# Kernel optimization log

Hardware: AMD Instinct MI355X
Metric: run time of the kernel (lower is better)

The kernel has to match this reference:

```python
import jax, jax.numpy as jnp
import numpy as np

NEG_SLOPE_GAT = 0.2    # PyG GATConv default negative_slope
NEG_SLOPE_ACT = 0.01   # F.leaky_relu default
D_DIRECTIONS = 4       # len(target): message directions per variable (uniform in this setup)
GAT_HEADS = 4


def gru_cell(x, h, Wih, Whh, bih, bhh):
    # torch.nn.GRUCell math; Wih [3H, in], Whh [3H, H]
    gi = x @ Wih.T + bih
    gh = h @ Whh.T + bhh
    ir, iz, inn = jnp.split(gi, 3, axis=1)
    hr, hz, hn = jnp.split(gh, 3, axis=1)
    r = jax.nn.sigmoid(ir + hr)
    z = jax.nn.sigmoid(iz + hz)
    n = jnp.tanh(inn + r * hn)
    return (1.0 - z) * n + z * h


def gat_conv(x, W, a_src, a_dst, bias, src, dst, heads, concat):
    # PyG GATConv (self-loops already included in src/dst)
    N = x.shape[0]
    C = W.shape[1] // heads
    h = (x @ W).reshape(N, heads, C)
    as_ = jnp.einsum('nhc,hc->nh', h, a_src)
    ad = jnp.einsum('nhc,hc->nh', h, a_dst)
    e = jax.nn.leaky_relu(as_[src] + ad[dst], NEG_SLOPE_GAT)  # [E, heads]
    m = jax.ops.segment_max(e, dst, num_segments=N)
    ex = jnp.exp(e - m[dst])
    den = jax.ops.segment_sum(ex, dst, num_segments=N)
    alpha = ex / den[dst]
    out = jax.ops.segment_sum(h[src] * alpha[:, :, None], dst, num_segments=N)
    if concat:
        return out.reshape(N, heads * C) + bias
    return out.mean(axis=1) + bias


def setup_inputs():
    key = jax.random.key(0)
    ki = iter(jax.random.split(key, 64))
    nk = lambda: next(ki)
    Nx, A, B = 100000, 50000, 50000
    IC, PD = 16, 3
    GH = IC - PD  # gru hidden = 13
    E, M, G, L, H, OC = 2000000, 1024, 1024, 4, 4, 32
    Ntot = Nx + A + B

    def p(*shape):
        return jax.random.normal(nk(), shape, jnp.float32) * 0.05

    inp = {}
    inp['x'] = jax.random.normal(nk(), (Nx, IC), jnp.float32)
    inp['edge_index'] = jax.random.randint(nk(), (2, E), 0, Ntot)
    inp['ass_to_sum_msg'] = jax.random.normal(nk(), (A, 1), jnp.float32)
    inp['ass_to_sum_hidden'] = jax.random.normal(nk(), (A, GH), jnp.float32)
    inp['sum_to_ass_msg'] = jax.random.normal(nk(), (B, 1), jnp.float32)
    inp['sum_to_ass_hidden'] = jax.random.normal(nk(), (B, GH), jnp.float32)
    inp['prefix'] = jax.random.normal(nk(), (A + B, PD), jnp.float32)
    inp['function_node_idxes'] = jax.random.randint(nk(), (M,), 0, Ntot)
    # regularized neighbor_idx_info: group g has direction idx=group_idx[g], src list group_src[g]
    # with idx at position 0 (out_i == 0) and no other entry equal to idx.
    gidx = jax.random.randint(nk(), (G,), 0, M)
    gs = jax.random.randint(nk(), (G, L), 0, M)
    rest = jnp.where(gs[:, 1:] == gidx[:, None], (gidx[:, None] + 1) % M, gs[:, 1:])
    inp['group_idx'] = gidx
    inp['group_src'] = jnp.concatenate([gidx[:, None], rest], axis=1)
    # GRU params
    for g in ('gru1', 'gru2'):
        inp[g + '_Wih'] = p(3 * GH, 1)
        inp[g + '_Whh'] = p(3 * GH, GH)
        inp[g + '_bih'] = p(3 * GH)
        inp[g + '_bhh'] = p(3 * GH)
    # GATConv params (W stored [in, heads*out], used as x @ W)
    inp['W1'] = p(IC, 32); inp['asrc1'] = p(4, 8); inp['adst1'] = p(4, 8); inp['b1'] = p(32)
    inp['W2'] = p(32, 32); inp['asrc2'] = p(4, 8); inp['adst2'] = p(4, 8); inp['b2'] = p(32)
    inp['W3'] = p(32, 32); inp['asrc3'] = p(4, 8); inp['adst3'] = p(4, 8); inp['b3'] = p(32)
    inp['W4'] = p(32, 4 * OC); inp['asrc4'] = p(4, OC); inp['adst4'] = p(4, OC); inp['b4'] = p(OC)
    # Attention heads: Wq/Wk [H, OC, OC] (applied as v @ Wq[h]), Ws [H, 2*OC], bs [H]
    inp['Wq'] = p(H, OC, OC); inp['Wk'] = p(H, OC, OC); inp['Ws'] = p(H, 2 * OC); inp['bs'] = p(H)
    return inp


def reference(x, edge_index, ass_to_sum_msg, ass_to_sum_hidden, sum_to_ass_msg,
              sum_to_ass_hidden, prefix, function_node_idxes, group_idx, group_src,
              gru1_Wih, gru1_Whh, gru1_bih, gru1_bhh,
              gru2_Wih, gru2_Whh, gru2_bih, gru2_bhh,
              W1, asrc1, adst1, b1, W2, asrc2, adst2, b2,
              W3, asrc3, adst3, b3, W4, asrc4, adst4, b4,
              Wq, Wk, Ws, bs):
    h1 = gru_cell(ass_to_sum_msg, ass_to_sum_hidden, gru1_Wih, gru1_Whh, gru1_bih, gru1_bhh)
    h2 = gru_cell(sum_to_ass_msg, sum_to_ass_hidden, gru2_Wih, gru2_Whh, gru2_bih, gru2_bhh)
    hidden = jnp.concatenate([h1, h2], axis=0)
    hidden = jnp.concatenate([prefix, hidden], axis=1)
    xx = jnp.concatenate([x, hidden], axis=0)
    N = xx.shape[0]
    loop = jnp.arange(N)
    src = jnp.concatenate([edge_index[0], loop])  # add self loops (PyG default)
    dst = jnp.concatenate([edge_index[1], loop])
    xx = jax.nn.leaky_relu(gat_conv(xx, W1, asrc1, adst1, b1, src, dst, GAT_HEADS, True), NEG_SLOPE_ACT)
    xx = jax.nn.leaky_relu(gat_conv(xx, W2, asrc2, adst2, b2, src, dst, GAT_HEADS, True), NEG_SLOPE_ACT)
    xx = jax.nn.leaky_relu(gat_conv(xx, W3, asrc3, adst3, b3, src, dst, GAT_HEADS, True), NEG_SLOPE_ACT)
    xx = jax.nn.leaky_relu(gat_conv(xx, W4, asrc4, adst4, b4, src, dst, GAT_HEADS, False), NEG_SLOPE_ACT)
    pooling = xx[function_node_idxes]  # [M, OC]
    hdim = pooling.shape[1]
    # score(i,j,h) = sigmoid((pooling_i @ Wq_h) . ws_q_h + (pooling_j @ Wk_h) . ws_k_h + bs_h)
    # (associativity: equals sigmoid(score_proj(cat([q_proj, k_proj]))) of the original)
    Vq = jnp.einsum('hdo,ho->hd', Wq, Ws[:, :hdim])
    Vk = jnp.einsum('hdo,ho->hd', Wk, Ws[:, hdim:])
    sq = pooling @ Vq.T  # [M, H]
    sk = pooling @ Vk.T  # [M, H]
    scores = jax.nn.sigmoid(sq[:, None, :] + sk[None, :, :] + bs)  # [M, M, H]; flat n -> (n//M, n%M)
    idx = group_idx
    nbr = group_src[:, 1:]  # idx itself sits at position 0 and is removed
    gathered = scores[idx[:, None], nbr]  # [G, L-1, H]
    trg = scores[idx, idx]                # [G, H]
    score_sum = gathered.mean(axis=1)
    tw = jax.nn.softmax(jnp.stack([score_sum, trg], axis=0), axis=0)  # [2, G, H]
    w = jax.nn.softmax(gathered, axis=1) * tw[0][:, None, :] * (D_DIRECTIONS - 1)
    weights = jnp.concatenate([tw[1][:, None, :], w], axis=1)  # [G, L, H] (out_i == 0)
    return weights, h1, h2
```

## Files before the change

### kernel.cpp

```cpp
#include <hip/hip_runtime.h>
#include <hip/hip_bf16.h>

#define NXD   100000
#define AROWS 50000
#define NND   200000
#define EED   2000000
#define ETOT  2200000
#define GHD   13
#define MMD   1024

#define OUT_H1 16384
#define OUT_H2 (16384 + AROWS * GHD)

#define NB    196
#define BSH   10
#define CAP   16000
#define TILE  4096

#define PREP_BIN   538
#define PREP_ASM   7422
#define PREP_GRU   392
#define FEAT_BLK   1563

typedef __hip_bfloat16 bf16;
typedef unsigned int uvec4 __attribute__((ext_vector_type(4)));

__device__ __forceinline__ float bf2f(bf16 v) { return __bfloat162float(v); }
__device__ __forceinline__ float sigm(float x) { return 1.f / (1.f + __expf(-x)); }
__device__ __forceinline__ float tanhfast(float x) {
    x = fminf(15.f, fmaxf(-15.f, x));
    float t = __expf(-2.f * x);
    return (1.f - t) / (1.f + t);
}
__device__ __forceinline__ float lrelu(float x, float s) { return x > 0.f ? x : s * x; }

__device__ __forceinline__ unsigned short f2bf_bits(float v) {
    bf16 b = __float2bfloat16(v);
    return *reinterpret_cast<unsigned short*>(&b);
}
__device__ __forceinline__ float bflo(unsigned int u) { return __uint_as_float((u & 0xFFFFu) << 16); }
__device__ __forceinline__ float bfhi(unsigned int u) { return __uint_as_float(u & 0xFFFF0000u); }

__device__ __forceinline__ float loadF(const void* p, size_t i, int f32) {
    return f32 ? ((const float*)p)[i] : bf2f(((const bf16*)p)[i]);
}
__device__ __forceinline__ void storeF(void* p, size_t i, float v, int f32) {
    if (f32) ((float*)p)[i] = v;
    else ((bf16*)p)[i] = __float2bfloat16(v);
}

__device__ __forceinline__ int flag_from_x(const void* xp, int tid, int* fl) {
    if (tid < 64) {
        const unsigned short* u = (const unsigned short*)xp;
        unsigned short b = u[tid * 2];
        int e = (b >> 7) & 0xFF;
        int viol = (e == 0xFF) || (e < 64) || (e > 190);
        unsigned long long mask = __ballot(viol != 0);
        if (tid == 0) *fl = (__popcll(mask) > 8) ? 1 : 0;
    }
    __syncthreads();
    return *fl;
}

__global__ void prep_kernel(const void* __restrict__ x, const void* __restrict__ prefix,
                            const void* __restrict__ msg1, const void* __restrict__ hid1,
                            const void* __restrict__ Wih1, const void* __restrict__ Whh1,
                            const void* __restrict__ bih1, const void* __restrict__ bhh1,
                            const void* __restrict__ msg2, const void* __restrict__ hid2,
                            const void* __restrict__ Wih2, const void* __restrict__ Whh2,
                            const void* __restrict__ bih2, const void* __restrict__ bhh2,
                            void* __restrict__ dout, bf16* __restrict__ bufA,
                            const int* __restrict__ src_e, const int* __restrict__ dst_e,
                            int* __restrict__ gtail, unsigned int* __restrict__ stage) {
    __shared__ int hist[NB];
    __shared__ int base[NB];
    __shared__ int cur[NB];
    __shared__ float WhhL[39 * 13], WihL[39], bihL[39], bhhL[39];
    __shared__ int fl;
    int bid = blockIdx.x, tid = threadIdx.x;
    if (bid < PREP_BIN) {
        for (int i = tid; i < NB; i += 256) hist[i] = 0;
        __syncthreads();
        int t0 = bid * TILE;
        int tend = t0 + TILE; if (tend > ETOT) tend = ETOT;
        for (int t = t0 + tid; t < tend; t += 256) {
            int d = (t < EED) ? dst_e[t] : (t - EED);
            atomicAdd(&hist[d >> BSH], 1);
        }
        __syncthreads();
        for (int i = tid; i < NB; i += 256) {
            int c = hist[i];
            base[i] = (c > 0) ? atomicAdd(&gtail[i], c) : 0;
            cur[i] = 0;
        }
        __syncthreads();
        for (int t = t0 + tid; t < tend; t += 256) {
            int s, d;
            if (t < EED) { s = src_e[t]; d = dst_e[t]; } else { s = d = t - EED; }
            int b = d >> BSH;
            int p = base[b] + atomicAdd(&cur[b], 1);
            if (p < CAP)
                stage[(size_t)b * CAP + p] = ((unsigned int)(d & 1023) << 18) | (unsigned int)s;
        }
    } else if (bid < PREP_BIN + PREP_ASM) {
        int f = flag_from_x(x, tid, &fl);
        int t = (bid - PREP_BIN) * 256 + tid;
        if (t < NXD * 16) {
            bufA[t] = __float2bfloat16(loadF(x, t, f));
        } else {
            int u = t - NXD * 16;
            if (u < NXD * 3) {
                int r = u / 3, c = u - r * 3;
                bufA[(size_t)(NXD + r) * 16 + c] = __float2bfloat16(loadF(prefix, u, f));
            }
        }
    } else {
        int f = flag_from_x(x, tid, &fl);
        int vb = bid - PREP_BIN - PREP_ASM;
        int which = vb >= 196;
        const void* msg = which ? msg2 : msg1;
        const void* hid = which ? hid2 : hid1;
        const void* Wih = which ? Wih2 : Wih1;
        const void* Whh = which ? Whh2 : Whh1;
        const void* bih = which ? bih2 : bih1;
        const void* bhh = which ? bhh2 : bhh1;
        size_t houtbase = which ? (size_t)OUT_H2 : (size_t)OUT_H1;
        int rowbase = which ? AROWS : 0;
        int blk = vb - (which ? 196 : 0);
        for (int i = tid; i < 39 * 13; i += 256) WhhL[i] = loadF(Whh, i, f);
        if (tid < 39) { WihL[tid] = loadF(Wih, tid, f); bihL[tid] = loadF(bih, tid, f); bhhL[tid] = loadF(bhh, tid, f); }
        __syncthreads();
        int n = blk * 256 + tid;
        if (n >= AROWS) return;
        float xv = loadF(msg, n, f);
        float h[GHD];
#pragma unroll
        for (int k = 0; k < GHD; k++) h[k] = loadF(hid, n * GHD + k, f);
#pragma unroll
        for (int k = 0; k < GHD; k++) {
            float gir = fmaf(xv, WihL[k],      bihL[k]);
            float giz = fmaf(xv, WihL[13 + k], bihL[13 + k]);
            float gin = fmaf(xv, WihL[26 + k], bihL[26 + k]);
            float ghr = bhhL[k], ghz = bhhL[13 + k], ghn = bhhL[26 + k];
#pragma unroll
            for (int q = 0; q < GHD; q++) {
                ghr = fmaf(h[q], WhhL[k * 13 + q],        ghr);
                ghz = fmaf(h[q], WhhL[(13 + k) * 13 + q], ghz);
                ghn = fmaf(h[q], WhhL[(26 + k) * 13 + q], ghn);
            }
            float r = sigm(gir + ghr);
            float z = sigm(giz + ghz);
            float nn = tanhfast(gin + r * ghn);
            float o = (1.f - z) * nn + z * h[k];
            storeF(dout, houtbase + (size_t)n * GHD + k, o, f);
            bufA[(size_t)(NXD + rowbase + n) * 16 + 3 + k] = __float2bfloat16(o);
        }
    }
}

template <int K>
__device__ __forceinline__ void feat_body(const bf16* __restrict__ xx,
                                          const void* __restrict__ W,
                                          bf16* __restrict__ hbuf, int f,
                                          int vbid, int tid) {
    int j = tid & 31;
    float Wc[K];
#pragma unroll
    for (int k = 0; k < K; k++) Wc[k] = loadF(W, k * 32 + j, f);
    int half = vbid * 8 + (tid >> 5);
    if (half >= NND / 16) return;
    int n0 = half * 16;
#pragma unroll 4
    for (int n = n0; n < n0 + 16; n++) {
        const uvec4* xr4 = (const uvec4*)(xx + (size_t)n * K);
        float v = 0.f;
#pragma unroll
        for (int q = 0; q < K / 8; q++) {
            uvec4 u = xr4[q];
            v = fmaf(bflo(u.x), Wc[q * 8 + 0], v);
            v = fmaf(bfhi(u.x), Wc[q * 8 + 1], v);
            v = fmaf(bflo(u.y), Wc[q * 8 + 2], v);
            v = fmaf(bfhi(u.y), Wc[q * 8 + 3], v);
            v = fmaf(bflo(u.z), Wc[q * 8 + 4], v);
            v = fmaf(bfhi(u.z), Wc[q * 8 + 5], v);
            v = fmaf(bflo(u.w), Wc[q * 8 + 6], v);
            v = fmaf(bfhi(u.w), Wc[q * 8 + 7], v);
        }
        hbuf[(size_t)n * 32 + j] = __float2bfloat16(v);
    }
}

__global__ void mid_kernel(const unsigned int* __restrict__ stage, const int* __restrict__ gtail,
                           int* __restrict__ offs, int* __restrict__ csr, int* __restrict__ order,
                           const bf16* __restrict__ xx, const void* __restrict__ W,
                           bf16* __restrict__ hbuf, const void* __restrict__ x) {
    __shared__ int cnt[1024];
    __shared__ int loc[1024];
    __shared__ int cur[1024];
    __shared__ int lds[256];
    __shared__ int dh[64];
    __shared__ int fl;
    int bid = blockIdx.x, tid = threadIdx.x;
    if (bid >= NB) {
        int f = flag_from_x(x, tid, &fl);
        feat_body<16>(xx, W, hbuf, f, bid - NB, tid);
        return;
    }
    int b = bid;
    int v = (tid < NB) ? gtail[tid] : 0;
    lds[tid] = v; __syncthreads();
    for (int off = 1; off < 256; off <<= 1) {
        int t2 = (tid >= off) ? lds[tid - off] : 0;
        __syncthreads();
        lds[tid] += t2;
        __syncthreads();
    }
    __shared__ int ebs;
    if (tid == b) ebs = lds[tid] - v;
    __syncthreads();
    int eb = ebs;
    int nE = gtail[b]; if (nE > CAP) nE = CAP;
    const unsigned int* st = stage + (size_t)b * CAP;
    for (int i = tid; i < 1024; i += 256) cnt[i] = 0;
    __syncthreads();
    for (int i = tid; i < nE; i += 256)
        atomicAdd(&cnt[st[i] >> 18], 1);
    __syncthreads();
    int c0 = cnt[tid * 4], c1 = cnt[tid * 4 + 1], c2 = cnt[tid * 4 + 2], c3 = cnt[tid * 4 + 3];
    int s = c0 + c1 + c2 + c3;
    lds[tid] = s; __syncthreads();
    for (int off = 1; off < 256; off <<= 1) {
        int t2 = (tid >= off) ? lds[tid - off] : 0;
        __syncthreads();
        lds[tid] += t2;
        __syncthreads();
    }
    int run = lds[tid] - s;
    loc[tid * 4]     = run;
    loc[tid * 4 + 1] = run + c0;
    loc[tid * 4 + 2] = run + c0 + c1;
    loc[tid * 4 + 3] = run + c0 + c1 + c2;
    __syncthreads();
    int nodebase = b << BSH;
    int bcnt = NND - nodebase; if (bcnt > 1024) bcnt = 1024;
    for (int i = tid; i < 1024; i += 256) {
        cur[i] = loc[i];
        int n = nodebase + i;
        if (n < NND) offs[n] = eb + loc[i];
    }
    if (b == 0 && tid == 0) offs[NND] = ETOT;
    if (tid < 64) dh[tid] = 0;
    __syncthreads();
    for (int i = tid; i < nE; i += 256) {
        unsigned int e = st[i];
        int dl = e >> 18;
        int src = e & 0x3FFFF;
        int p = atomicAdd(&cur[dl], 1);
        csr[eb + p] = src;
    }
    for (int i = tid; i < bcnt; i += 256) {
        int dcl = cnt[i]; if (dcl > 63) dcl = 63;
        atomicAdd(&dh[dcl], 1);
    }
    __syncthreads();
    if (tid == 0) {
        int acc = 0;
        for (int k = 0; k < 64; k++) { int c = dh[k]; dh[k] = acc; acc += c; }
    }
    __syncthreads();
    for (int i = tid; i < bcnt; i += 256) {
        int dcl = cnt[i]; if (dcl > 63) dcl = 63;
        int pos = atomicAdd(&dh[dcl], 1);
        order[nodebase + pos] = nodebase + i;
    }
}

template <int K>
__global__ void feat_kernel(const bf16* __restrict__ xx, const void* __restrict__ W,
                            bf16* __restrict__ hbuf, const void* __restrict__ x) {
    __shared__ int fl;
    int tid = threadIdx.x;
    int f = flag_from_x(x, tid, &fl);
    feat_body<K>(xx, W, hbuf, f, blockIdx.x, tid);
}

__global__ void agg_kernel(const bf16* __restrict__ hbuf, const int* __restrict__ offs,
                           const int* __restrict__ csr, const int* __restrict__ order,
                           const void* __restrict__ asrc, const void* __restrict__ adst,
                           const void* __restrict__ bias, bf16* __restrict__ xxout,
                           const void* __restrict__ x) {
    __shared__ float bl[32], asl[32], adl[32];
    __shared__ int fl;
    int tid = threadIdx.x;
    int f = flag_from_x(x, tid, &fl);
    if (tid < 32) {
        bl[tid]  = loadF(bias, tid, f);
        asl[tid] = loadF(asrc, tid, f);
        adl[tid] = loadF(adst, tid, f);
    }
    __syncthreads();
    int n = order[blockIdx.x * 64 + (tid >> 2)];
    int j = tid & 3;
    int cb = 8 * j;
    float A0 = asl[cb], A1 = asl[cb + 1], A2 = asl[cb + 2], A3 = asl[cb + 3];
    float A4 = asl[cb + 4], A5 = asl[cb + 5], A6 = asl[cb + 6], A7 = asl[cb + 7];
    uvec4 hd = *(const uvec4*)(hbuf + (size_t)n * 32 + cb);
    float adv = bflo(hd.x) * adl[cb]     + bfhi(hd.x) * adl[cb + 1]
              + bflo(hd.y) * adl[cb + 2] + bfhi(hd.y) * adl[cb + 3]
              + bflo(hd.z) * adl[cb + 4] + bfhi(hd.z) * adl[cb + 5]
              + bflo(hd.w) * adl[cb + 6] + bfhi(hd.w) * adl[cb + 7];
    int beg = offs[n], end = offs[n + 1];
    int cnt = end - beg;
    const int* cp = csr + beg;
    uvec4 h0 = *(const uvec4*)(hbuf + (size_t)cp[0] * 32 + cb);
    uvec4 h1 = h0, h2 = h0;
    if (cnt > 1) h1 = *(const uvec4*)(hbuf + (size_t)cp[1] * 32 + cb);
    if (cnt > 2) h2 = *(const uvec4*)(hbuf + (size_t)cp[2] * 32 + cb);
    float den = 0.f;
    float a0 = 0.f, a1 = 0.f, a2 = 0.f, a3 = 0.f, a4 = 0.f, a5 = 0.f, a6 = 0.f, a7 = 0.f;
    for (int i = 0; i < cnt; i++) {
        uvec4 hn = (uvec4)(0u);
        if (i + 3 < cnt) {
            int sn = cp[i + 3];
            hn = *(const uvec4*)(hbuf + (size_t)sn * 32 + cb);
        }
        float v0 = bflo(h0.x), v1 = bfhi(h0.x), v2 = bflo(h0.y), v3 = bfhi(h0.y);
        float v4 = bflo(h0.z), v5 = bfhi(h0.z), v6 = bflo(h0.w), v7 = bfhi(h0.w);
        float as = v0 * A0 + v1 * A1 + v2 * A2 + v3 * A3
                 + v4 * A4 + v5 * A5 + v6 * A6 + v7 * A7;
        float e = as + adv;
        e = e > 0.f ? e : 0.2f * e;
        e = fminf(50.f, fmaxf(-50.f, e));
        float w = __expf(e);
        den += w;
        a0 = fmaf(w, v0, a0); a1 = fmaf(w, v1, a1);
        a2 = fmaf(w, v2, a2); a3 = fmaf(w, v3, a3);
        a4 = fmaf(w, v4, a4); a5 = fmaf(w, v5, a5);
        a6 = fmaf(w, v6, a6); a7 = fmaf(w, v7, a7);
        h0 = h1; h1 = h2; h2 = hn;
    }
    float inv = 1.f / den;
    float o0 = lrelu(fmaf(a0, inv, bl[cb + 0]), 0.01f);
    float o1 = lrelu(fmaf(a1, inv, bl[cb + 1]), 0.01f);
    float o2 = lrelu(fmaf(a2, inv, bl[cb + 2]), 0.01f);
    float o3 = lrelu(fmaf(a3, inv, bl[cb + 3]), 0.01f);
    float o4 = lrelu(fmaf(a4, inv, bl[cb + 4]), 0.01f);
    float o5 = lrelu(fmaf(a5, inv, bl[cb + 5]), 0.01f);
    float o6 = lrelu(fmaf(a6, inv, bl[cb + 6]), 0.01f);
    float o7 = lrelu(fmaf(a7, inv, bl[cb + 7]), 0.01f);
    uvec4 p;
    p.x = ((unsigned int)f2bf_bits(o1) << 16) | f2bf_bits(o0);
    p.y = ((unsigned int)f2bf_bits(o3) << 16) | f2bf_bits(o2);
    p.z = ((unsigned int)f2bf_bits(o5) << 16) | f2bf_bits(o4);
    p.w = ((unsigned int)f2bf_bits(o7) << 16) | f2bf_bits(o6);
    __builtin_nontemporal_store(p, (uvec4*)(xxout + (size_t)n * 32 + cb));
}

__global__ void layer4_kernel(const bf16* __restrict__ xx,
                              const void* __restrict__ W4,
                              const void* __restrict__ asrc,
                              const void* __restrict__ adst,
                              const void* __restrict__ b4,
                              const int* __restrict__ fidx, const int* __restrict__ offs,
                              const int* __restrict__ csr, float* __restrict__ pool,
                              const void* __restrict__ x) {
    __shared__ float Wl[32 * 128];
    __shared__ float asl[128], adl[128], bl[32];
    __shared__ float accs[4][32];
    __shared__ float dens[4];
    __shared__ int fl;
    int tid = threadIdx.x;
    int f = flag_from_x(x, tid, &fl);
    for (int i = tid; i < 32 * 128; i += 256) Wl[i] = loadF(W4, i, f);
    if (tid < 128) { asl[tid] = loadF(asrc, tid, f); adl[tid] = loadF(adst, tid, f); accs[tid >> 5][tid & 31] = 0.f; }
    if (tid < 32) bl[tid] = loadF(b4, tid, f);
    if (tid < 4) dens[tid] = 0.f;
    __syncthreads();
    int g = blockIdx.x;
    int d = fidx[g];
    int wave = tid >> 6, lane = tid & 63;
    int c = lane & 31;
    int h0 = lane >> 5;
    int h1 = h0 + 2;
    const uvec4* xd4 = (const uvec4*)(xx + (size_t)d * 32);
    uvec4 du0 = xd4[0], du1 = xd4[1];
    float v0 = 0.f, v1 = 0.f;
    {
        unsigned int us[8] = {du0.x, du0.y, du0.z, du0.w, du1.x, du1.y, du1.z, du1.w};
#pragma unroll
        for (int q = 0; q < 8; q++) {
            unsigned int u = us[q];
            int k = 2 * q;
            v0 = fmaf(bflo(u), Wl[k * 128 + lane], v0);       v0 = fmaf(bfhi(u), Wl[(k + 1) * 128 + lane], v0);
            v1 = fmaf(bflo(u), Wl[k * 128 + lane + 64], v1);  v1 = fmaf(bfhi(u), Wl[(k + 1) * 128 + lane + 64], v1);
        }
    }
    float ad0 = v0 * adl[h0 * 32 + c];
    float ad1 = v1 * adl[h1 * 32 + c];
#pragma unroll
    for (int mk = 1; mk < 32; mk <<= 1) { ad0 += __shfl_xor(ad0, mk); ad1 += __shfl_xor(ad1, mk); }
    int beg = offs[d], end = offs[d + 1];
    float den0 = 0.f, den1 = 0.f, acc0 = 0.f, acc1 = 0.f;
    for (int i = beg + wave; i < end; i += 4) {
        int s = csr[i];
        const uvec4* xs4 = (const uvec4*)(xx + (size_t)s * 32);
        uvec4 su0 = xs4[0], su1 = xs4[1];
        float s0 = 0.f, s1 = 0.f;
        unsigned int us[8] = {su0.x, su0.y, su0.z, su0.w, su1.x, su1.y, su1.z, su1.w};
#pragma unroll
        for (int q = 0; q < 8; q++) {
            unsigned int u = us[q];
            int k = 2 * q;
            s0 = fmaf(bflo(u), Wl[k * 128 + lane], s0);       s0 = fmaf(bfhi(u), Wl[(k + 1) * 128 + lane], s0);
            s1 = fmaf(bflo(u), Wl[k * 128 + lane + 64], s1);  s1 = fmaf(bfhi(u), Wl[(k + 1) * 128 + lane + 64], s1);
        }
        float as0 = s0 * asl[h0 * 32 + c];
        float as1 = s1 * asl[h1 * 32 + c];
#pragma unroll
        for (int mk = 1; mk < 32; mk <<= 1) { as0 += __shfl_xor(as0, mk); as1 += __shfl_xor(as1, mk); }
        float e0 = lrelu(as0 + ad0, 0.2f);
        float e1 = lrelu(as1 + ad1, 0.2f);
        e0 = fminf(50.f, fmaxf(-50.f, e0));
        e1 = fminf(50.f, fmaxf(-50.f, e1));
        float w0 = __expf(e0), w1 = __expf(e1);
        den0 += w0; acc0 = fmaf(w0, s0, acc0);
        den1 += w1; acc1 = fmaf(w1, s1, acc1);
    }
    atomicAdd(&accs[h0][c], acc0);
    atomicAdd(&accs[h1][c], acc1);
    if (c == 0) { atomicAdd(&dens[h0], den0); atomicAdd(&dens[h1], den1); }
    __syncthreads();
    if (tid < 32) {
        float t = accs[0][tid] / dens[0] + accs[1][tid] / dens[1]
                + accs[2][tid] / dens[2] + accs[3][tid] / dens[3];
        float o = t * 0.25f + bl[tid];
        pool[g * 32 + tid] = lrelu(o, 0.01f);
    }
}

__global__ void tail_kernel(const void* __restrict__ Wq, const void* __restrict__ Wk,
                            const void* __restrict__ Ws, const void* __restrict__ bs,
                            const int* __restrict__ gidx, const int* __restrict__ gsrc,
                            const float* __restrict__ pool, void* __restrict__ out,
                            const void* __restrict__ x) {
    __shared__ float vq[128], vk[128];
    __shared__ float sq[4096], sk[4096];
    __shared__ int fl;
    int tid = threadIdx.x;
    int f = flag_from_x(x, tid, &fl);
    {
        int which = tid >> 7;
        int i = tid & 127;
        int h = i >> 5, dd = i & 31;
        const void* Wm = which ? Wk : Wq;
        float sum = 0.f;
#pragma unroll
        for (int o = 0; o < 32; o++)
            sum = fmaf(loadF(Wm, (h * 32 + dd) * 32 + o, f), loadF(Ws, h * 64 + which * 32 + o, f), sum);
        (which ? vk : vq)[i] = sum;
    }
    __syncthreads();
    for (int idx = tid; idx < 8192; idx += 256) {
        int which = idx >> 12;
        int i = idx & 4095;
        int g = i >> 2, h = i & 3;
        const float* V = which ? vk : vq;
        float s = 0.f;
#pragma unroll
        for (int dd = 0; dd < 32; dd++) s = fmaf(pool[g * 32 + dd], V[h * 32 + dd], s);
        (which ? sk : sq)[i] = s;
    }
    __syncthreads();
    for (int t = tid; t < 4096; t += 256) {
        int g = t >> 2, h = t & 3;
        int i = gidx[g];
        float bsv = loadF(bs, h, f);
        float sqi = sq[i * 4 + h];
        float trg = sigm(sqi + sk[i * 4 + h] + bsv);
        float ga[3];
#pragma unroll
        for (int q = 0; q < 3; q++) {
            int jj = gsrc[g * 4 + 1 + q];
            ga[q] = sigm(sqi + sk[jj * 4 + h] + bsv);
        }
        float ss = (ga[0] + ga[1] + ga[2]) * (1.f / 3.f);
        float mx = fmaxf(ss, trg);
        float e0 = __expf(ss - mx), e1 = __expf(trg - mx);
        float inv = 1.f / (e0 + e1);
        float tw0 = e0 * inv, tw1 = e1 * inv;
        float mg = fmaxf(ga[0], fmaxf(ga[1], ga[2]));
        float w0 = __expf(ga[0] - mg), w1 = __expf(ga[1] - mg), w2 = __expf(ga[2] - mg);
        float wi = tw0 * 3.f / (w0 + w1 + w2);
        storeF(out, g * 16 + 0 + h,  tw1,     f);
        storeF(out, g * 16 + 4 + h,  w0 * wi, f);
        storeF(out, g * 16 + 8 + h,  w1 * wi, f);
        storeF(out, g * 16 + 12 + h, w2 * wi, f);
    }
}

extern "C" void kernel_launch(void* const* d_in, const int* in_sizes, int n_in,
                              void* d_out, int out_size, void* d_ws, size_t ws_size,
                              hipStream_t stream) {
    const void* x        = d_in[0];
    const int*  ei       = (const int*)d_in[1];
    const void* a2s_msg  = d_in[2];
    const void* a2s_hid  = d_in[3];
    const void* s2a_msg  = d_in[4];
    const void* s2a_hid  = d_in[5];
    const void* prefix   = d_in[6];
    const int*  fidx     = (const int*)d_in[7];
    const int*  gidx     = (const int*)d_in[8];
    const int*  gsrc     = (const int*)d_in[9];
    const void* g1_Wih   = d_in[10];
    const void* g1_Whh   = d_in[11];
    const void* g1_bih   = d_in[12];
    const void* g1_bhh   = d_in[13];
    const void* g2_Wih   = d_in[14];
    const void* g2_Whh   = d_in[15];
    const void* g2_bih   = d_in[16];
    const void* g2_bhh   = d_in[17];
    const void* W1  = d_in[18];
    const void* as1 = d_in[19];
    const void* ad1 = d_in[20];
    const void* b1  = d_in[21];
    const void* W2  = d_in[22];
    const void* as2 = d_in[23];
    const void* ad2 = d_in[24];
    const void* b2  = d_in[25];
    const void* W3  = d_in[26];
    const void* as3 = d_in[27];
    const void* ad3 = d_in[28];
    const void* b3  = d_in[29];
    const void* W4  = d_in[30];
    const void* as4 = d_in[31];
    const void* ad4 = d_in[32];
    const void* b4  = d_in[33];
    const void* Wq  = d_in[34];
    const void* Wk  = d_in[35];
    const void* Ws  = d_in[36];
    const void* bs  = d_in[37];

    const int* src_e = ei;
    const int* dst_e = ei + EED;

    char* wp = (char*)d_ws;
    auto alloc = [&](size_t bytes) {
        char* p = wp;
        wp += (bytes + 255) & ~(size_t)255;
        return p;
    };
    int*   csr   = (int*)alloc((size_t)ETOT * 4);
    int*   offs  = (int*)alloc((size_t)(NND + 1) * 4);
    int*   order = (int*)alloc((size_t)NND * 4);
    int*   gtail = (int*)alloc((size_t)NB * 4);
    float* pool  = (float*)alloc((size_t)MMD * 32 * 4);
    bf16*  bufA  = (bf16*)alloc((size_t)NND * 32 * 2);
    bf16*  bufB  = (bf16*)alloc((size_t)NND * 32 * 2);
    unsigned int* stage = (unsigned int*)alloc((size_t)NB * CAP * 4);

    hipMemsetAsync(gtail, 0, (size_t)NB * 4, stream);
    prep_kernel<<<PREP_BIN + PREP_ASM + PREP_GRU, 256, 0, stream>>>(
        x, prefix,
        a2s_msg, a2s_hid, g1_Wih, g1_Whh, g1_bih, g1_bhh,
        s2a_msg, s2a_hid, g2_Wih, g2_Whh, g2_bih, g2_bhh,
        d_out, bufA, src_e, dst_e, gtail, stage);

    mid_kernel<<<NB + FEAT_BLK, 256, 0, stream>>>(stage, gtail, offs, csr, order,
                                                  bufA, W1, bufB, x);

    const int nblk_agg = NND / 64;
    agg_kernel<<<nblk_agg, 256, 0, stream>>>(bufB, offs, csr, order, as1, ad1, b1, bufA, x);
    feat_kernel<32><<<FEAT_BLK, 256, 0, stream>>>(bufA, W2, bufB, x);
    agg_kernel<<<nblk_agg, 256, 0, stream>>>(bufB, offs, csr, order, as2, ad2, b2, bufA, x);
    feat_kernel<32><<<FEAT_BLK, 256, 0, stream>>>(bufA, W3, bufB, x);
    agg_kernel<<<nblk_agg, 256, 0, stream>>>(bufB, offs, csr, order, as3, ad3, b3, bufA, x);

    layer4_kernel<<<MMD, 256, 0, stream>>>(bufA, W4, as4, ad4, b4, fidx, offs, csr, pool, x);
    tail_kernel<<<1, 256, 0, stream>>>(Wq, Wk, Ws, bs, gidx, gsrc, pool, d_out, x);
}
```

Measured before the change: 496.9 us.

## Split prep kernel, drop degree ordering, shorten prefetch, add launch bounds in aggregation

```diff
diff --git a/kernel.cpp b/kernel.cpp
--- a/kernel.cpp
+++ b/kernel.cpp
@@ -17,9 +17,8 @@
 #define CAP   16000
 #define TILE  4096
 
-#define PREP_BIN   538
-#define PREP_ASM   7422
-#define PREP_GRU   392
+#define ASM_BLK    7422
+#define GRU_BLK    392
 #define FEAT_BLK   1563
 
 typedef __hip_bfloat16 bf16;
@@ -62,49 +61,51 @@
     return *fl;
 }
 
-__global__ void prep_kernel(const void* __restrict__ x, const void* __restrict__ prefix,
-                            const void* __restrict__ msg1, const void* __restrict__ hid1,
-                            const void* __restrict__ Wih1, const void* __restrict__ Whh1,
-                            const void* __restrict__ bih1, const void* __restrict__ bhh1,
-                            const void* __restrict__ msg2, const void* __restrict__ hid2,
-                            const void* __restrict__ Wih2, const void* __restrict__ Whh2,
-                            const void* __restrict__ bih2, const void* __restrict__ bhh2,
-                            void* __restrict__ dout, bf16* __restrict__ bufA,
-                            const int* __restrict__ src_e, const int* __restrict__ dst_e,
-                            int* __restrict__ gtail, unsigned int* __restrict__ stage) {
+__global__ void bin_kernel(const int* __restrict__ src_e, const int* __restrict__ dst_e,
+                           int* __restrict__ gtail, unsigned int* __restrict__ stage) {
     __shared__ int hist[NB];
     __shared__ int base[NB];
     __shared__ int cur[NB];
+    int tid = threadIdx.x;
+    for (int i = tid; i < NB; i += 256) hist[i] = 0;
+    __syncthreads();
+    int t0 = blockIdx.x * TILE;
+    int tend = t0 + TILE; if (tend > ETOT) tend = ETOT;
+    for (int t = t0 + tid; t < tend; t += 256) {
+        int d = (t < EED) ? dst_e[t] : (t - EED);
+        atomicAdd(&hist[d >> BSH], 1);
+    }
+    __syncthreads();
+    for (int i = tid; i < NB; i += 256) {
+        int c = hist[i];
+        base[i] = (c > 0) ? atomicAdd(&gtail[i], c) : 0;
+        cur[i] = 0;
+    }
+    __syncthreads();
+    for (int t = t0 + tid; t < tend; t += 256) {
+        int s, d;
+        if (t < EED) { s = src_e[t]; d = dst_e[t]; } else { s = d = t - EED; }
+        int b = d >> BSH;
+        int p = base[b] + atomicAdd(&cur[b], 1);
+        if (p < CAP)
+            stage[(size_t)b * CAP + p] = ((unsigned int)(d & 1023) << 18) | (unsigned int)s;
+    }
+}
+
+__global__ void asmgru_kernel(const void* __restrict__ x, const void* __restrict__ prefix,
+                              const void* __restrict__ msg1, const void* __restrict__ hid1,
+                              const void* __restrict__ Wih1, const void* __restrict__ Whh1,
+                              const void* __restrict__ bih1, const void* __restrict__ bhh1,
+                              const void* __restrict__ msg2, const void* __restrict__ hid2,
+                              const void* __restrict__ Wih2, const void* __restrict__ Whh2,
+                              const void* __restrict__ bih2, const void* __restrict__ bhh2,
+                              void* __restrict__ dout, bf16* __restrict__ bufA) {
     __shared__ float WhhL[39 * 13], WihL[39], bihL[39], bhhL[39];
     __shared__ int fl;
     int bid = blockIdx.x, tid = threadIdx.x;
-    if (bid < PREP_BIN) {
-        for (int i = tid; i < NB; i += 256) hist[i] = 0;
-        __syncthreads();
-        int t0 = bid * TILE;
-        int tend = t0 + TILE; if (tend > ETOT) tend = ETOT;
-        for (int t = t0 + tid; t < tend; t += 256) {
-            int d = (t < EED) ? dst_e[t] : (t - EED);
-            atomicAdd(&hist[d >> BSH], 1);
-        }
-        __syncthreads();
-        for (int i = tid; i < NB; i += 256) {
-            int c = hist[i];
-            base[i] = (c > 0) ? atomicAdd(&gtail[i], c) : 0;
-            cur[i] = 0;
-        }
-        __syncthreads();
-        for (int t = t0 + tid; t < tend; t += 256) {
-            int s, d;
-            if (t < EED) { s = src_e[t]; d = dst_e[t]; } else { s = d = t - EED; }
-            int b = d >> BSH;
-            int p = base[b] + atomicAdd(&cur[b], 1);
-            if (p < CAP)
-                stage[(size_t)b * CAP + p] = ((unsigned int)(d & 1023) << 18) | (unsigned int)s;
-        }
-    } else if (bid < PREP_BIN + PREP_ASM) {
-        int f = flag_from_x(x, tid, &fl);
-        int t = (bid - PREP_BIN) * 256 + tid;
+    int f = flag_from_x(x, tid, &fl);
+    if (bid < ASM_BLK) {
+        int t = bid * 256 + tid;
         if (t < NXD * 16) {
             bufA[t] = __float2bfloat16(loadF(x, t, f));
         } else {
@@ -114,47 +115,46 @@
                 bufA[(size_t)(NXD + r) * 16 + c] = __float2bfloat16(loadF(prefix, u, f));
             }
         }
-    } else {
-        int f = flag_from_x(x, tid, &fl);
-        int vb = bid - PREP_BIN - PREP_ASM;
-        int which = vb >= 196;
-        const void* msg = which ? msg2 : msg1;
-        const void* hid = which ? hid2 : hid1;
-        const void* Wih = which ? Wih2 : Wih1;
-        const void* Whh = which ? Whh2 : Whh1;
-        const void* bih = which ? bih2 : bih1;
-        const void* bhh = which ? bhh2 : bhh1;
-        size_t houtbase = which ? (size_t)OUT_H2 : (size_t)OUT_H1;
-        int rowbase = which ? AROWS : 0;
-        int blk = vb - (which ? 196 : 0);
-        for (int i = tid; i < 39 * 13; i += 256) WhhL[i] = loadF(Whh, i, f);
-        if (tid < 39) { WihL[tid] = loadF(Wih, tid, f); bihL[tid] = loadF(bih, tid, f); bhhL[tid] = loadF(bhh, tid, f); }
-        __syncthreads();
-        int n = blk * 256 + tid;
-        if (n >= AROWS) return;
-        float xv = loadF(msg, n, f);
-        float h[GHD];
-#pragma unroll
-        for (int k = 0; k < GHD; k++) h[k] = loadF(hid, n * GHD + k, f);
-#pragma unroll
-        for (int k = 0; k < GHD; k++) {
-            float gir = fmaf(xv, WihL[k],      bihL[k]);
-            float giz = fmaf(xv, WihL[13 + k], bihL[13 + k]);
-            float gin = fmaf(xv, WihL[26 + k], bihL[26 + k]);
-            float ghr = bhhL[k], ghz = bhhL[13 + k], ghn = bhhL[26 + k];
-#pragma unroll
-            for (int q = 0; q < GHD; q++) {
-                ghr = fmaf(h[q], WhhL[k * 13 + q],        ghr);
-                ghz = fmaf(h[q], WhhL[(13 + k) * 13 + q], ghz);
-                ghn = fmaf(h[q], WhhL[(26 + k) * 13 + q], ghn);
-            }
-            float r = sigm(gir + ghr);
-            float z = sigm(giz + ghz);
-            float nn = tanhfast(gin + r * ghn);
-            float o = (1.f - z) * nn + z * h[k];
-            storeF(dout, houtbase + (size_t)n * GHD + k, o, f);
-            bufA[(size_t)(NXD + rowbase + n) * 16 + 3 + k] = __float2bfloat16(o);
-        }
+        return;
+    }
+    int vb = bid - ASM_BLK;
+    int which = vb >= 196;
+    const void* msg = which ? msg2 : msg1;
+    const void* hid = which ? hid2 : hid1;
+    const void* Wih = which ? Wih2 : Wih1;
+    const void* Whh = which ? Whh2 : Whh1;
+    const void* bih = which ? bih2 : bih1;
+    const void* bhh = which ? bhh2 : bhh1;
+    size_t houtbase = which ? (size_t)OUT_H2 : (size_t)OUT_H1;
+    int rowbase = which ? AROWS : 0;
+    int blk = vb - (which ? 196 : 0);
+    for (int i = tid; i < 39 * 13; i += 256) WhhL[i] = loadF(Whh, i, f);
+    if (tid < 39) { WihL[tid] = loadF(Wih, tid, f); bihL[tid] = loadF(bih, tid, f); bhhL[tid] = loadF(bhh, tid, f); }
+    __syncthreads();
+    int n = blk * 256 + tid;
+    if (n >= AROWS) return;
+    float xv = loadF(msg, n, f);
+    float h[GHD];
+#pragma unroll
+    for (int k = 0; k < GHD; k++) h[k] = loadF(hid, n * GHD + k, f);
+#pragma unroll
+    for (int k = 0; k < GHD; k++) {
+        float gir = fmaf(xv, WihL[k],      bihL[k]);
+        float giz = fmaf(xv, WihL[13 + k], bihL[13 + k]);
+        float gin = fmaf(xv, WihL[26 + k], bihL[26 + k]);
+        float ghr = bhhL[k], ghz = bhhL[13 + k], ghn = bhhL[26 + k];
+#pragma unroll
+        for (int q = 0; q < GHD; q++) {
+            ghr = fmaf(h[q], WhhL[k * 13 + q],        ghr);
+            ghz = fmaf(h[q], WhhL[(13 + k) * 13 + q], ghz);
+            ghn = fmaf(h[q], WhhL[(26 + k) * 13 + q], ghn);
+        }
+        float r = sigm(gir + ghr);
+        float z = sigm(giz + ghz);
+        float nn = tanhfast(gin + r * ghn);
+        float o = (1.f - z) * nn + z * h[k];
+        storeF(dout, houtbase + (size_t)n * GHD + k, o, f);
+        bufA[(size_t)(NXD + rowbase + n) * 16 + 3 + k] = __float2bfloat16(o);
     }
 }
 
@@ -191,14 +191,13 @@
 }
 
 __global__ void mid_kernel(const unsigned int* __restrict__ stage, const int* __restrict__ gtail,
-                           int* __restrict__ offs, int* __restrict__ csr, int* __restrict__ order,
+                           int* __restrict__ offs, int* __restrict__ csr,
                            const bf16* __restrict__ xx, const void* __restrict__ W,
                            bf16* __restrict__ hbuf, const void* __restrict__ x) {
     __shared__ int cnt[1024];
     __shared__ int loc[1024];
     __shared__ int cur[1024];
     __shared__ int lds[256];
-    __shared__ int dh[64];
     __shared__ int fl;
     int bid = blockIdx.x, tid = threadIdx.x;
     if (bid >= NB) {
@@ -242,14 +241,12 @@
     loc[tid * 4 + 3] = run + c0 + c1 + c2;
     __syncthreads();
     int nodebase = b << BSH;
-    int bcnt = NND - nodebase; if (bcnt > 1024) bcnt = 1024;
     for (int i = tid; i < 1024; i += 256) {
         cur[i] = loc[i];
         int n = nodebase + i;
         if (n < NND) offs[n] = eb + loc[i];
     }
     if (b == 0 && tid == 0) offs[NND] = ETOT;
-    if (tid < 64) dh[tid] = 0;
     __syncthreads();
     for (int i = tid; i < nE; i += 256) {
         unsigned int e = st[i];
@@ -257,21 +254,6 @@
         int src = e & 0x3FFFF;
         int p = atomicAdd(&cur[dl], 1);
         csr[eb + p] = src;
-    }
-    for (int i = tid; i < bcnt; i += 256) {
-        int dcl = cnt[i]; if (dcl > 63) dcl = 63;
-        atomicAdd(&dh[dcl], 1);
-    }
-    __syncthreads();
-    if (tid == 0) {
-        int acc = 0;
-        for (int k = 0; k < 64; k++) { int c = dh[k]; dh[k] = acc; acc += c; }
-    }
-    __syncthreads();
-    for (int i = tid; i < bcnt; i += 256) {
-        int dcl = cnt[i]; if (dcl > 63) dcl = 63;
-        int pos = atomicAdd(&dh[dcl], 1);
-        order[nodebase + pos] = nodebase + i;
     }
 }
 
@@ -284,11 +266,11 @@
     feat_body<K>(xx, W, hbuf, f, blockIdx.x, tid);
 }
 
-__global__ void agg_kernel(const bf16* __restrict__ hbuf, const int* __restrict__ offs,
-                           const int* __restrict__ csr, const int* __restrict__ order,
-                           const void* __restrict__ asrc, const void* __restrict__ adst,
-                           const void* __restrict__ bias, bf16* __restrict__ xxout,
-                           const void* __restrict__ x) {
+__global__ void __launch_bounds__(256, 8)
+agg_kernel(const bf16* __restrict__ hbuf, const int* __restrict__ offs,
+           const int* __restrict__ csr, const void* __restrict__ asrc,
+           const void* __restrict__ adst, const void* __restrict__ bias,
+           bf16* __restrict__ xxout, const void* __restrict__ x) {
     __shared__ float bl[32], asl[32], adl[32];
     __shared__ int fl;
     int tid = threadIdx.x;
@@ -299,7 +281,7 @@
         adl[tid] = loadF(adst, tid, f);
     }
     __syncthreads();
-    int n = order[blockIdx.x * 64 + (tid >> 2)];
+    int n = blockIdx.x * 64 + (tid >> 2);
     int j = tid & 3;
     int cb = 8 * j;
     float A0 = asl[cb], A1 = asl[cb + 1], A2 = asl[cb + 2], A3 = asl[cb + 3];
@@ -313,15 +295,14 @@
     int cnt = end - beg;
     const int* cp = csr + beg;
     uvec4 h0 = *(const uvec4*)(hbuf + (size_t)cp[0] * 32 + cb);
-    uvec4 h1 = h0, h2 = h0;
+    uvec4 h1 = h0;
     if (cnt > 1) h1 = *(const uvec4*)(hbuf + (size_t)cp[1] * 32 + cb);
-    if (cnt > 2) h2 = *(const uvec4*)(hbuf + (size_t)cp[2] * 32 + cb);
     float den = 0.f;
     float a0 = 0.f, a1 = 0.f, a2 = 0.f, a3 = 0.f, a4 = 0.f, a5 = 0.f, a6 = 0.f, a7 = 0.f;
     for (int i = 0; i < cnt; i++) {
         uvec4 hn = (uvec4)(0u);
-        if (i + 3 < cnt) {
-            int sn = cp[i + 3];
+        if (i + 2 < cnt) {
+            int sn = cp[i + 2];
             hn = *(const uvec4*)(hbuf + (size_t)sn * 32 + cb);
         }
         float v0 = bflo(h0.x), v1 = bfhi(h0.x), v2 = bflo(h0.y), v3 = bfhi(h0.y);
@@ -337,7 +318,7 @@
         a2 = fmaf(w, v2, a2); a3 = fmaf(w, v3, a3);
         a4 = fmaf(w, v4, a4); a5 = fmaf(w, v5, a5);
         a6 = fmaf(w, v6, a6); a7 = fmaf(w, v7, a7);
-        h0 = h1; h1 = h2; h2 = hn;
+        h0 = h1; h1 = hn;
     }
     float inv = 1.f / den;
     float o0 = lrelu(fmaf(a0, inv, bl[cb + 0]), 0.01f);
@@ -551,7 +532,6 @@
     };
     int*   csr   = (int*)alloc((size_t)ETOT * 4);
     int*   offs  = (int*)alloc((size_t)(NND + 1) * 4);
-    int*   order = (int*)alloc((size_t)NND * 4);
     int*   gtail = (int*)alloc((size_t)NB * 4);
     float* pool  = (float*)alloc((size_t)MMD * 32 * 4);
     bf16*  bufA  = (bf16*)alloc((size_t)NND * 32 * 2);
@@ -559,21 +539,21 @@
     unsigned int* stage = (unsigned int*)alloc((size_t)NB * CAP * 4);
 
     hipMemsetAsync(gtail, 0, (size_t)NB * 4, stream);
-    prep_kernel<<<PREP_BIN + PREP_ASM + PREP_GRU, 256, 0, stream>>>(
+    bin_kernel<<<(ETOT + TILE - 1) / TILE, 256, 0, stream>>>(src_e, dst_e, gtail, stage);
+    asmgru_kernel<<<ASM_BLK + GRU_BLK, 256, 0, stream>>>(
         x, prefix,
         a2s_msg, a2s_hid, g1_Wih, g1_Whh, g1_bih, g1_bhh,
         s2a_msg, s2a_hid, g2_Wih, g2_Whh, g2_bih, g2_bhh,
-        d_out, bufA, src_e, dst_e, gtail, stage);
-
-    mid_kernel<<<NB + FEAT_BLK, 256, 0, stream>>>(stage, gtail, offs, csr, order,
-                                                  bufA, W1, bufB, x);
+        d_out, bufA);
+
+    mid_kernel<<<NB + FEAT_BLK, 256, 0, stream>>>(stage, gtail, offs, csr, bufA, W1, bufB, x);
 
     const int nblk_agg = NND / 64;
-    agg_kernel<<<nblk_agg, 256, 0, stream>>>(bufB, offs, csr, order, as1, ad1, b1, bufA, x);
+    agg_kernel<<<nblk_agg, 256, 0, stream>>>(bufB, offs, csr, as1, ad1, b1, bufA, x);
     feat_kernel<32><<<FEAT_BLK, 256, 0, stream>>>(bufA, W2, bufB, x);
-    agg_kernel<<<nblk_agg, 256, 0, stream>>>(bufB, offs, csr, order, as2, ad2, b2, bufA, x);
+    agg_kernel<<<nblk_agg, 256, 0, stream>>>(bufB, offs, csr, as2, ad2, b2, bufA, x);
     feat_kernel<32><<<FEAT_BLK, 256, 0, stream>>>(bufA, W3, bufB, x);
-    agg_kernel<<<nblk_agg, 256, 0, stream>>>(bufB, offs, csr, order, as3, ad3, b3, bufA, x);
+    agg_kernel<<<nblk_agg, 256, 0, stream>>>(bufB, offs, csr, as3, ad3, b3, bufA, x);
 
     layer4_kernel<<<MMD, 256, 0, stream>>>(bufA, W4, as4, ad4, b4, fidx, offs, csr, pool, x);
     tail_kernel<<<1, 256, 0, stream>>>(Wq, Wk, Ws, bs, gidx, gsrc, pool, d_out, x);
```

After: 446.2 us. 10.2% less time.
